# Performance work log

Hardware: AMD Instinct MI355X
Metric: run time of the kernel (lower is better)

Reference implementation:

```python
import jax, jax.numpy as jnp
import numpy as np

H = 12      # num_attention_heads
DH = 64     # attention_head_size
D = H * DH  # hidden_size = 768
EPS = 1e-12

def setup_inputs() -> dict:
    key = jax.random.key(0)
    ks = jax.random.split(key, 12)
    B, S = 8, 1024
    s = 0.02
    return {
        "hidden_states": jax.random.normal(ks[0], (B, S, D), jnp.float32),
        "attention_mask": jnp.zeros((B, 1, 1, S), jnp.float32),
        "Wq": jax.random.normal(ks[1], (D, D), jnp.float32) * s,
        "bq": jnp.zeros((D,), jnp.float32),
        "Wk": jax.random.normal(ks[2], (D, D), jnp.float32) * s,
        "bk": jnp.zeros((D,), jnp.float32),
        "Wv": jax.random.normal(ks[3], (D, D), jnp.float32) * s,
        "bv": jnp.zeros((D,), jnp.float32),
        "Wd": jax.random.normal(ks[4], (D, D), jnp.float32) * s,
        "bd": jnp.zeros((D,), jnp.float32),
        "ln_g": jnp.ones((D,), jnp.float32),
        "ln_b": jnp.zeros((D,), jnp.float32),
    }

def _heads(x, W, b):
    # [B,S,D] -> [B,H,S,Dh]
    B, S, _ = x.shape
    y = x @ W.T + b
    return y.reshape(B, S, H, DH).transpose(0, 2, 1, 3)

def reference(hidden_states, attention_mask, Wq, bq, Wk, bk, Wv, bv, Wd, bd, ln_g, ln_b):
    q = _heads(hidden_states, Wq, bq)
    k = _heads(hidden_states, Wk, bk)
    v = _heads(hidden_states, Wv, bv)
    scores = jnp.einsum('bhqd,bhkd->bhqk', q, k) / np.sqrt(DH).astype(np.float32)
    scores = scores + attention_mask  # broadcast [B,1,1,S]
    probs = jax.nn.softmax(scores, axis=-1)
    ctx = jnp.einsum('bhqk,bhkd->bhqd', probs, v)
    B, _, S, _ = ctx.shape
    ctx = ctx.transpose(0, 2, 1, 3).reshape(B, S, D)
    out = ctx @ Wd.T + bd  # dropout = identity (eval)
    x = hidden_states + out
    mu = jnp.mean(x, axis=-1, keepdims=True)
    var = jnp.var(x, axis=-1, keepdims=True)
    return (x - mu) / jnp.sqrt(var + EPS) * ln_g + ln_b
```

## Files before the change

kernel.cpp:

```cpp
#include <hip/hip_runtime.h>

typedef unsigned short u16;
typedef unsigned int u32;

#define H_ 12
#define DH_ 64
#define D_ 768
#define S_ 1024
#define B_ 8
#define M_TOT 8192
#define LOG2E 1.44269504089f

using f32x4  = __attribute__((ext_vector_type(4))) float;
using bf16x8 = __attribute__((ext_vector_type(8))) short;

__device__ inline u16 f2bf(float f) {
  union { float f; u32 u; } v; v.f = f;
  u32 r = v.u + 0x7FFFu + ((v.u >> 16) & 1u);
  return (u16)(r >> 16);
}

__device__ inline float bf2f(u16 b) {
  union { u32 u; float f; } v; v.u = ((u32)b) << 16;
  return v.f;
}

__device__ inline void gload_lds16(const u16* g, u16* l) {
  __builtin_amdgcn_global_load_lds((const __attribute__((address_space(1))) void*)g,
                                   (__attribute__((address_space(3))) void*)l, 16, 0, 0);
}

__global__ void convert_all(const float* __restrict__ X,
                            const float* __restrict__ Wq, const float* __restrict__ Wk,
                            const float* __restrict__ Wv, const float* __restrict__ Wd,
                            u16* __restrict__ Xb, u16* __restrict__ Wqkv, u16* __restrict__ Wdb) {
  int stride = gridDim.x * blockDim.x;
  int tid = blockIdx.x * blockDim.x + threadIdx.x;
  const int NX4 = M_TOT * D_ / 4;
  const int NW4 = D_ * D_ / 4;
  const int NW = D_ * D_;
  for (int i = tid; i < NX4; i += stride) {
    float4 x = ((const float4*)X)[i];
    uint2 p;
    p.x = (u32)f2bf(x.x) | ((u32)f2bf(x.y) << 16);
    p.y = (u32)f2bf(x.z) | ((u32)f2bf(x.w) << 16);
    ((uint2*)Xb)[i] = p;
  }
  for (int i = tid; i < NW4; i += stride) {
    float4 q = ((const float4*)Wq)[i];
    float4 k = ((const float4*)Wk)[i];
    float4 v = ((const float4*)Wv)[i];
    float4 d = ((const float4*)Wd)[i];
    uint2 pq, pk, pv, pd;
    pq.x = (u32)f2bf(q.x) | ((u32)f2bf(q.y) << 16); pq.y = (u32)f2bf(q.z) | ((u32)f2bf(q.w) << 16);
    pk.x = (u32)f2bf(k.x) | ((u32)f2bf(k.y) << 16); pk.y = (u32)f2bf(k.z) | ((u32)f2bf(k.w) << 16);
    pv.x = (u32)f2bf(v.x) | ((u32)f2bf(v.y) << 16); pv.y = (u32)f2bf(v.z) | ((u32)f2bf(v.w) << 16);
    pd.x = (u32)f2bf(d.x) | ((u32)f2bf(d.y) << 16); pd.y = (u32)f2bf(d.z) | ((u32)f2bf(d.w) << 16);
    ((uint2*)Wqkv)[i]            = pq;
    ((uint2*)(Wqkv + NW))[i]     = pk;
    ((uint2*)(Wqkv + 2*NW))[i]   = pv;
    ((uint2*)Wdb)[i]             = pd;
  }
}

#define NT_ 24

__global__ __launch_bounds__(256, 4) void gemm_qkv(
    const u16* __restrict__ A, const u16* __restrict__ Bw,
    const float* __restrict__ bq, const float* __restrict__ bk, const float* __restrict__ bv,
    u16* __restrict__ Q, u16* __restrict__ K, u16* __restrict__ Vt) {
  __shared__ u16 As[2 * 128 * 32];
  __shared__ u16 Bs[2 * 128 * 32];
  int tid = threadIdx.x, lane = tid & 63, wave = tid >> 6;
  int wg = blockIdx.x;
  int xcd = wg & 7, li = wg >> 3;
  int m0 = (xcd * 8 + (li & 7)) * 128;
  int n0 = (li >> 3) * 128;
  int wm = (wave >> 1) * 64, wn = (wave & 1) * 64;
  int fr = lane & 15, fg = lane >> 4;
  f32x4 acc[4][4] = {};

  int srow = tid >> 2;
  int schunk = (lane & 3) ^ ((lane >> 3) & 3);
  const u16* AgS = A  + (size_t)(m0 + srow) * D_ + schunk * 8;
  const u16* BgS = Bw + (size_t)(n0 + srow) * D_ + schunk * 8;
  u16* Abase = &As[wave * 512];
  u16* Bbase = &Bs[wave * 512];
  int ra = (fg ^ ((fr >> 1) & 3)) * 8;

  gload_lds16(AgS,            Abase);
  gload_lds16(AgS + 64 * D_,  Abase + 2048);
  gload_lds16(BgS,            Bbase);
  gload_lds16(BgS + 64 * D_,  Bbase + 2048);
  __syncthreads();

  for (int t = 0; t < NT_; ++t) {
    int cur = t & 1, nxt = cur ^ 1;
    if (t < NT_ - 1) {
      int k1 = (t + 1) * 32;
      gload_lds16(AgS + k1,           Abase + nxt * 4096);
      gload_lds16(AgS + 64 * D_ + k1, Abase + nxt * 4096 + 2048);
      gload_lds16(BgS + k1,           Bbase + nxt * 4096);
      gload_lds16(BgS + 64 * D_ + k1, Bbase + nxt * 4096 + 2048);
    }
    bf16x8 af[4], bf[4];
#pragma unroll
    for (int i = 0; i < 4; i++) {
      af[i] = *(const bf16x8*)&As[cur * 4096 + (wm + i * 16 + fr) * 32 + ra];
      bf[i] = *(const bf16x8*)&Bs[cur * 4096 + (wn + i * 16 + fr) * 32 + ra];
    }
    __builtin_amdgcn_s_setprio(1);
#pragma unroll
    for (int mi = 0; mi < 4; mi++)
#pragma unroll
      for (int ni = 0; ni < 4; ni++)
        acc[mi][ni] = __builtin_amdgcn_mfma_f32_16x16x32_bf16(af[mi], bf[ni], acc[mi][ni], 0, 0, 0);
    __builtin_amdgcn_s_setprio(0);
    __syncthreads();
  }

  int which = n0 / D_;
  int ncol0 = n0 % D_;
  const float* bias = (which == 0) ? bq : (which == 1) ? bk : bv;
  if (which == 2) {
#pragma unroll
    for (int mi = 0; mi < 4; mi++)
#pragma unroll
      for (int ni = 0; ni < 4; ni++) {
        int col = ncol0 + wn + ni*16 + fr;
        float bb = bias[col];
        int row = m0 + wm + mi*16 + fg*4;
        int bidx = row >> 10, s = row & 1023;
        int hh = col >> 6, dd = col & 63;
        u16 t0 = f2bf(acc[mi][ni][0] + bb);
        u16 t1 = f2bf(acc[mi][ni][1] + bb);
        u16 t2 = f2bf(acc[mi][ni][2] + bb);
        u16 t3 = f2bf(acc[mi][ni][3] + bb);
        uint2 pk2;
        pk2.x = (u32)t0 | ((u32)t1 << 16);
        pk2.y = (u32)t2 | ((u32)t3 << 16);
        *(uint2*)(Vt + ((size_t)((bidx * H_ + hh) * DH_ + dd)) * S_ + s) = pk2;
      }
  } else {
    u16* Out = (which == 0) ? Q : K;
    float scale = (which == 0) ? (0.125f * LOG2E) : 1.0f;
#pragma unroll
    for (int mi = 0; mi < 4; mi++)
#pragma unroll
      for (int ni = 0; ni < 4; ni++) {
        int col = ncol0 + wn + ni*16 + fr;
        float bb = bias[col];
#pragma unroll
        for (int r = 0; r < 4; r++) {
          int row = m0 + wm + mi*16 + fg*4 + r;
          Out[row * D_ + col] = f2bf((acc[mi][ni][r] + bb) * scale);
        }
      }
  }
}

__global__ __launch_bounds__(256, 4) void gemm_out(
    const u16* __restrict__ A, const u16* __restrict__ Bw,
    const float* __restrict__ bd, const float* __restrict__ hidden,
    u16* __restrict__ Tmp) {
  __shared__ u16 As[2 * 64 * 32];
  __shared__ u16 Bs[2 * 128 * 32];
  int tid = threadIdx.x, lane = tid & 63, wave = tid >> 6;
  int wg = blockIdx.x;
  int xcd = wg & 7, li = wg >> 3;
  int m0 = (xcd * 16 + (li & 15)) * 64;
  int n0 = (li >> 4) * 128;
  int wm = (wave >> 1) * 32, wn = (wave & 1) * 64;
  int fr = lane & 15, fg = lane >> 4;
  f32x4 acc[2][4] = {};

  int srow = tid >> 2;
  int schunk = (lane & 3) ^ ((lane >> 3) & 3);
  const u16* AgS = A  + (size_t)(m0 + srow) * D_ + schunk * 8;
  const u16* BgS = Bw + (size_t)(n0 + srow) * D_ + schunk * 8;
  u16* Abase = &As[wave * 512];
  u16* Bbase = &Bs[wave * 512];
  int ra = (fg ^ ((fr >> 1) & 3)) * 8;

  gload_lds16(AgS,            Abase);
  gload_lds16(BgS,            Bbase);
  gload_lds16(BgS + 64 * D_,  Bbase + 2048);
  __syncthreads();

  for (int t = 0; t < NT_; ++t) {
    int cur = t & 1, nxt = cur ^ 1;
    if (t < NT_ - 1) {
      int k1 = (t + 1) * 32;
      gload_lds16(AgS + k1,           Abase + nxt * 2048);
      gload_lds16(BgS + k1,           Bbase + nxt * 4096);
      gload_lds16(BgS + 64 * D_ + k1, Bbase + nxt * 4096 + 2048);
    }
    bf16x8 af[2], bf[4];
#pragma unroll
    for (int i = 0; i < 2; i++)
      af[i] = *(const bf16x8*)&As[cur * 2048 + (wm + i * 16 + fr) * 32 + ra];
#pragma unroll
    for (int i = 0; i < 4; i++)
      bf[i] = *(const bf16x8*)&Bs[cur * 4096 + (wn + i * 16 + fr) * 32 + ra];
    __builtin_amdgcn_s_setprio(1);
#pragma unroll
    for (int mi = 0; mi < 2; mi++)
#pragma unroll
      for (int ni = 0; ni < 4; ni++)
        acc[mi][ni] = __builtin_amdgcn_mfma_f32_16x16x32_bf16(af[mi], bf[ni], acc[mi][ni], 0, 0, 0);
    __builtin_amdgcn_s_setprio(0);
    __syncthreads();
  }

#pragma unroll
  for (int mi = 0; mi < 2; mi++)
#pragma unroll
    for (int ni = 0; ni < 4; ni++) {
      int col = n0 + wn + ni*16 + fr;
      float bb = bd[col];
#pragma unroll
      for (int r = 0; r < 4; r++) {
        int row = m0 + wm + mi*16 + fg*4 + r;
        Tmp[row * D_ + col] = f2bf(acc[mi][ni][r] + bb + hidden[(size_t)row * D_ + col]);
      }
    }
}

__global__ __launch_bounds__(256) void attn_kernel(
    const u16* __restrict__ Q, const u16* __restrict__ K, const u16* __restrict__ Vt,
    const float* __restrict__ mask, u16* __restrict__ Ctx) {
  __shared__ u16 Ks[2][64 * 64];
  __shared__ u16 Vs[2][64 * 64];
  __shared__ u16 Ps[4][16 * 64];
  int tid = threadIdx.x, lane = tid & 63, wave = tid >> 6;
  int i = blockIdx.x;
  int xcd = i & 7, slot = i >> 3;
  int bh = xcd * 12 + (slot >> 3);
  int qt = slot & 7;
  int b = bh / H_, h = bh % H_;
  int q0 = qt * 128 + wave * 32;
  int fr = lane & 15, fg = lane >> 4;

  bf16x8 qf[2][2];
#pragma unroll
  for (int s = 0; s < 2; s++) {
    const u16* Qrow = Q + (size_t)(b * S_ + q0 + s*16 + fr) * D_ + h * DH_;
    qf[s][0] = *(const bf16x8*)(Qrow + fg * 8);
    qf[s][1] = *(const bf16x8*)(Qrow + 32 + fg * 8);
  }

  int srow = tid >> 2;
  int scc = (tid & 3) * 16;
  int sw = (srow & 7) << 3;
  int sidx0 = srow * 64 + (scc ^ sw);
  int sidx1 = srow * 64 + ((scc + 8) ^ sw);
  const u16* Kg0 = K  + (size_t)(b * S_ + srow) * D_ + h * DH_ + scc;
  const u16* Vg0 = Vt + (size_t)(bh * DH_ + srow) * S_ + scc;
  const float* mbase = mask + b * S_;

  int frw = (fr & 7) << 3;
  int rc0 = (fg * 8) ^ frw;
  int rc1 = (32 + fg * 8) ^ frw;
  int pcw[4];
#pragma unroll
  for (int kb = 0; kb < 4; kb++) pcw[kb] = (kb * 16 + fg * 4) ^ frw;

  f32x4 acc[2][4] = {};
  float l_part[2] = {0.f, 0.f};

  int4 kr0 = *(const int4*)Kg0;
  int4 kr1 = *(const int4*)(Kg0 + 8);
  int4 vr0 = *(const int4*)Vg0;
  int4 vr1 = *(const int4*)(Vg0 + 8);
  *(int4*)&Ks[0][sidx0] = kr0; *(int4*)&Ks[0][sidx1] = kr1;
  *(int4*)&Vs[0][sidx0] = vr0; *(int4*)&Vs[0][sidx1] = vr1;
  __syncthreads();

  u16* Pw = Ps[wave];

  for (int t = 0; t < 16; ++t) {
    int cur = t & 1;
    int kt = t * 64;
    if (t < 15) {
      const u16* Kg = Kg0 + (size_t)(kt + 64) * D_;
      const u16* Vg = Vg0 + (kt + 64);
      kr0 = *(const int4*)Kg; kr1 = *(const int4*)(Kg + 8);
      vr0 = *(const int4*)Vg; vr1 = *(const int4*)(Vg + 8);
    }

    f32x4 mv[4];
#pragma unroll
    for (int kb = 0; kb < 4; kb++) {
      float4 m4 = *(const float4*)&mbase[kt + kb*16 + fg*4];
      mv[kb][0] = m4.x * LOG2E; mv[kb][1] = m4.y * LOG2E;
      mv[kb][2] = m4.z * LOG2E; mv[kb][3] = m4.w * LOG2E;
    }

    bf16x8 kf[4][2];
#pragma unroll
    for (int kb = 0; kb < 4; kb++) {
      int r = kb * 16 + fr;
      kf[kb][0] = *(const bf16x8*)&Ks[cur][r * 64 + rc0];
      kf[kb][1] = *(const bf16x8*)&Ks[cur][r * 64 + rc1];
    }

    bf16x8 pf[2][2];
#pragma unroll
    for (int s = 0; s < 2; s++) {
#pragma unroll
      for (int kb = 0; kb < 4; kb++) {
        f32x4 sv = mv[kb];
        sv = __builtin_amdgcn_mfma_f32_16x16x32_bf16(kf[kb][0], qf[s][0], sv, 0, 0, 0);
        sv = __builtin_amdgcn_mfma_f32_16x16x32_bf16(kf[kb][1], qf[s][1], sv, 0, 0, 0);
        float p0 = __builtin_amdgcn_exp2f(sv[0]);
        float p1 = __builtin_amdgcn_exp2f(sv[1]);
        float p2 = __builtin_amdgcn_exp2f(sv[2]);
        float p3 = __builtin_amdgcn_exp2f(sv[3]);
        l_part[s] += (p0 + p1) + (p2 + p3);
        u32 lo, hi;
        asm("v_cvt_pk_bf16_f32 %0, %1, %2" : "=v"(lo) : "v"(p0), "v"(p1));
        asm("v_cvt_pk_bf16_f32 %0, %1, %2" : "=v"(hi) : "v"(p2), "v"(p3));
        uint2 pk2; pk2.x = lo; pk2.y = hi;
        *(uint2*)&Pw[fr * 64 + pcw[kb]] = pk2;
      }
      pf[s][0] = *(const bf16x8*)&Pw[fr * 64 + rc0];
      pf[s][1] = *(const bf16x8*)&Pw[fr * 64 + rc1];
    }

    __builtin_amdgcn_s_setprio(1);
#pragma unroll
    for (int ns = 0; ns < 4; ns++) {
      int r = ns * 16 + fr;
      bf16x8 vf0 = *(const bf16x8*)&Vs[cur][r * 64 + rc0];
      bf16x8 vf1 = *(const bf16x8*)&Vs[cur][r * 64 + rc1];
#pragma unroll
      for (int s = 0; s < 2; s++) {
        acc[s][ns] = __builtin_amdgcn_mfma_f32_16x16x32_bf16(pf[s][0], vf0, acc[s][ns], 0, 0, 0);
        acc[s][ns] = __builtin_amdgcn_mfma_f32_16x16x32_bf16(pf[s][1], vf1, acc[s][ns], 0, 0, 0);
      }
    }
    __builtin_amdgcn_s_setprio(0);

    if (t < 15) {
      int nxt = cur ^ 1;
      *(int4*)&Ks[nxt][sidx0] = kr0; *(int4*)&Ks[nxt][sidx1] = kr1;
      *(int4*)&Vs[nxt][sidx0] = vr0; *(int4*)&Vs[nxt][sidx1] = vr1;
      __syncthreads();
    }
  }

  float li[2][4];
#pragma unroll
  for (int s = 0; s < 2; s++) {
    l_part[s] += __shfl_xor(l_part[s], 16);
    l_part[s] += __shfl_xor(l_part[s], 32);
    float inv = 1.0f / l_part[s];
#pragma unroll
    for (int r = 0; r < 4; r++)
      li[s][r] = __shfl(inv, fg*4 + r);
  }
#pragma unroll
  for (int s = 0; s < 2; s++) {
    u16* Crow = Ctx + (size_t)(b * S_ + q0 + s*16) * D_ + h * DH_;
#pragma unroll
    for (int ns = 0; ns < 4; ns++)
#pragma unroll
      for (int r = 0; r < 4; r++)
        Crow[(fg*4 + r) * D_ + ns*16 + fr] = f2bf(acc[s][ns][r] * li[s][r]);
  }
}

__global__ __launch_bounds__(256) void ln_kernel(
    const u16* __restrict__ Tmp, const float* __restrict__ g,
    const float* __restrict__ bta, float* __restrict__ out) {
  int wave = threadIdx.x >> 6, lane = threadIdx.x & 63;
  int row = blockIdx.x * 4 + wave;
  const uint2* x2 = (const uint2*)(Tmp + (size_t)row * D_);
  const float4* g4 = (const float4*)g;
  const float4* b4 = (const float4*)bta;
  float4* o4 = (float4*)(out + (size_t)row * D_);
  float v[3][4];
  float s = 0.f, s2 = 0.f;
#pragma unroll
  for (int w = 0; w < 3; w++) {
    uint2 raw = x2[lane + w * 64];
    v[w][0] = bf2f((u16)(raw.x & 0xFFFF));
    v[w][1] = bf2f((u16)(raw.x >> 16));
    v[w][2] = bf2f((u16)(raw.y & 0xFFFF));
    v[w][3] = bf2f((u16)(raw.y >> 16));
#pragma unroll
    for (int e = 0; e < 4; e++) { s += v[w][e]; s2 += v[w][e] * v[w][e]; }
  }
#pragma unroll
  for (int m = 1; m < 64; m <<= 1) { s += __shfl_xor(s, m); s2 += __shfl_xor(s2, m); }
  float mean = s * (1.0f / D_);
  float var = s2 * (1.0f / D_) - mean * mean;
  float inv = rsqrtf(var + 1e-12f);
#pragma unroll
  for (int w = 0; w < 3; w++) {
    float4 gg = g4[lane + w * 64];
    float4 bb = b4[lane + w * 64];
    float4 o;
    o.x = (v[w][0] - mean) * inv * gg.x + bb.x;
    o.y = (v[w][1] - mean) * inv * gg.y + bb.y;
    o.z = (v[w][2] - mean) * inv * gg.z + bb.z;
    o.w = (v[w][3] - mean) * inv * gg.w + bb.w;
    o4[lane + w * 64] = o;
  }
}

extern "C" void kernel_launch(void* const* d_in, const int* in_sizes, int n_in,
                              void* d_out, int out_size, void* d_ws, size_t ws_size,
                              hipStream_t stream) {
  (void)in_sizes; (void)n_in; (void)out_size; (void)ws_size;
  const float* hidden = (const float*)d_in[0];
  const float* mask   = (const float*)d_in[1];
  const float* Wq = (const float*)d_in[2];
  const float* bq = (const float*)d_in[3];
  const float* Wk = (const float*)d_in[4];
  const float* bk = (const float*)d_in[5];
  const float* Wv = (const float*)d_in[6];
  const float* bv = (const float*)d_in[7];
  const float* Wd = (const float*)d_in[8];
  const float* bd = (const float*)d_in[9];
  const float* ln_g = (const float*)d_in[10];
  const float* ln_b = (const float*)d_in[11];
  float* out = (float*)d_out;

  char* ws = (char*)d_ws;
  u16* Xb    = (u16*)(ws);
  u16* Wqkv  = (u16*)(ws + 12582912);
  u16* Wdb   = (u16*)(ws + 16121856);
  u16* Q     = (u16*)(ws + 17301504);
  u16* K     = (u16*)(ws + 29884416);
  u16* Vt    = (u16*)(ws + 42467328);
  u16* Ctx   = (u16*)(ws + 55050240);
  u16* Tmp   = (u16*)(ws + 17301504);

  convert_all<<<2048, 256, 0, stream>>>(hidden, Wq, Wk, Wv, Wd, Xb, Wqkv, Wdb);
  gemm_qkv<<<1152, 256, 0, stream>>>(Xb, Wqkv, bq, bk, bv, Q, K, Vt);
  attn_kernel<<<768, 256, 0, stream>>>(Q, K, Vt, mask, Ctx);
  gemm_out<<<768, 256, 0, stream>>>(Ctx, Wdb, bd, hidden, Tmp);
  ln_kernel<<<2048, 256, 0, stream>>>(Tmp, ln_g, ln_b, out);
}
```

Measured before the change: 127.9 us.

## Halve attention query tile per block and stage scaled mask in shared memory

Each attention block now handles 64 queries (16 per wave) instead of 128, doubling the grid to 1536 blocks for better occupancy and CU balance. The mask row is preloaded into shared memory once, pre-scaled by log2e, instead of being read from global each tile. The trade-off is that each block reuses its loaded K/V tiles for half as many queries, so total K/V global traffic doubles. Register pressure per wave drops, which may let more waves stay resident.

```diff
diff --git a/kernel.cpp b/kernel.cpp
--- a/kernel.cpp
+++ b/kernel.cpp
@@ -232,22 +232,25 @@
   __shared__ u16 Ks[2][64 * 64];
   __shared__ u16 Vs[2][64 * 64];
   __shared__ u16 Ps[4][16 * 64];
+  __shared__ float Ms[S_];
   int tid = threadIdx.x, lane = tid & 63, wave = tid >> 6;
   int i = blockIdx.x;
   int xcd = i & 7, slot = i >> 3;
-  int bh = xcd * 12 + (slot >> 3);
-  int qt = slot & 7;
+  int bh = xcd * 12 + (slot >> 4);
+  int qt = slot & 15;
   int b = bh / H_, h = bh % H_;
-  int q0 = qt * 128 + wave * 32;
+  int q0 = qt * 64 + wave * 16;
   int fr = lane & 15, fg = lane >> 4;
 
-  bf16x8 qf[2][2];
-#pragma unroll
-  for (int s = 0; s < 2; s++) {
-    const u16* Qrow = Q + (size_t)(b * S_ + q0 + s*16 + fr) * D_ + h * DH_;
-    qf[s][0] = *(const bf16x8*)(Qrow + fg * 8);
-    qf[s][1] = *(const bf16x8*)(Qrow + 32 + fg * 8);
-  }
+  {
+    float4 m4 = ((const float4*)(mask + b * S_))[tid];
+    m4.x *= LOG2E; m4.y *= LOG2E; m4.z *= LOG2E; m4.w *= LOG2E;
+    ((float4*)Ms)[tid] = m4;
+  }
+
+  const u16* Qrow = Q + (size_t)(b * S_ + q0 + fr) * D_ + h * DH_;
+  bf16x8 qf0 = *(const bf16x8*)(Qrow + fg * 8);
+  bf16x8 qf1 = *(const bf16x8*)(Qrow + 32 + fg * 8);
 
   int srow = tid >> 2;
   int scc = (tid & 3) * 16;
@@ -256,7 +259,6 @@
   int sidx1 = srow * 64 + ((scc + 8) ^ sw);
   const u16* Kg0 = K  + (size_t)(b * S_ + srow) * D_ + h * DH_ + scc;
   const u16* Vg0 = Vt + (size_t)(bh * DH_ + srow) * S_ + scc;
-  const float* mbase = mask + b * S_;
 
   int frw = (fr & 7) << 3;
   int rc0 = (fg * 8) ^ frw;
@@ -265,8 +267,8 @@
 #pragma unroll
   for (int kb = 0; kb < 4; kb++) pcw[kb] = (kb * 16 + fg * 4) ^ frw;
 
-  f32x4 acc[2][4] = {};
-  float l_part[2] = {0.f, 0.f};
+  f32x4 acc[4] = {};
+  float l_part = 0.f;
 
   int4 kr0 = *(const int4*)Kg0;
   int4 kr1 = *(const int4*)(Kg0 + 8);
@@ -288,44 +290,28 @@
       vr0 = *(const int4*)Vg; vr1 = *(const int4*)(Vg + 8);
     }
 
-    f32x4 mv[4];
-#pragma unroll
-    for (int kb = 0; kb < 4; kb++) {
-      float4 m4 = *(const float4*)&mbase[kt + kb*16 + fg*4];
-      mv[kb][0] = m4.x * LOG2E; mv[kb][1] = m4.y * LOG2E;
-      mv[kb][2] = m4.z * LOG2E; mv[kb][3] = m4.w * LOG2E;
-    }
-
-    bf16x8 kf[4][2];
 #pragma unroll
     for (int kb = 0; kb < 4; kb++) {
       int r = kb * 16 + fr;
-      kf[kb][0] = *(const bf16x8*)&Ks[cur][r * 64 + rc0];
-      kf[kb][1] = *(const bf16x8*)&Ks[cur][r * 64 + rc1];
-    }
-
-    bf16x8 pf[2][2];
-#pragma unroll
-    for (int s = 0; s < 2; s++) {
-#pragma unroll
-      for (int kb = 0; kb < 4; kb++) {
-        f32x4 sv = mv[kb];
-        sv = __builtin_amdgcn_mfma_f32_16x16x32_bf16(kf[kb][0], qf[s][0], sv, 0, 0, 0);
-        sv = __builtin_amdgcn_mfma_f32_16x16x32_bf16(kf[kb][1], qf[s][1], sv, 0, 0, 0);
-        float p0 = __builtin_amdgcn_exp2f(sv[0]);
-        float p1 = __builtin_amdgcn_exp2f(sv[1]);
-        float p2 = __builtin_amdgcn_exp2f(sv[2]);
-        float p3 = __builtin_amdgcn_exp2f(sv[3]);
-        l_part[s] += (p0 + p1) + (p2 + p3);
-        u32 lo, hi;
-        asm("v_cvt_pk_bf16_f32 %0, %1, %2" : "=v"(lo) : "v"(p0), "v"(p1));
-        asm("v_cvt_pk_bf16_f32 %0, %1, %2" : "=v"(hi) : "v"(p2), "v"(p3));
-        uint2 pk2; pk2.x = lo; pk2.y = hi;
-        *(uint2*)&Pw[fr * 64 + pcw[kb]] = pk2;
-      }
-      pf[s][0] = *(const bf16x8*)&Pw[fr * 64 + rc0];
-      pf[s][1] = *(const bf16x8*)&Pw[fr * 64 + rc1];
-    }
+      bf16x8 kf0 = *(const bf16x8*)&Ks[cur][r * 64 + rc0];
+      bf16x8 kf1 = *(const bf16x8*)&Ks[cur][r * 64 + rc1];
+      float4 m4 = *(const float4*)&Ms[kt + kb*16 + fg*4];
+      f32x4 sv; sv[0] = m4.x; sv[1] = m4.y; sv[2] = m4.z; sv[3] = m4.w;
+      sv = __builtin_amdgcn_mfma_f32_16x16x32_bf16(kf0, qf0, sv, 0, 0, 0);
+      sv = __builtin_amdgcn_mfma_f32_16x16x32_bf16(kf1, qf1, sv, 0, 0, 0);
+      float p0 = __builtin_amdgcn_exp2f(sv[0]);
+      float p1 = __builtin_amdgcn_exp2f(sv[1]);
+      float p2 = __builtin_amdgcn_exp2f(sv[2]);
+      float p3 = __builtin_amdgcn_exp2f(sv[3]);
+      l_part += (p0 + p1) + (p2 + p3);
+      u32 lo, hi;
+      asm("v_cvt_pk_bf16_f32 %0, %1, %2" : "=v"(lo) : "v"(p0), "v"(p1));
+      asm("v_cvt_pk_bf16_f32 %0, %1, %2" : "=v"(hi) : "v"(p2), "v"(p3));
+      uint2 pk2; pk2.x = lo; pk2.y = hi;
+      *(uint2*)&Pw[fr * 64 + pcw[kb]] = pk2;
+    }
+    bf16x8 pf0 = *(const bf16x8*)&Pw[fr * 64 + rc0];
+    bf16x8 pf1 = *(const bf16x8*)&Pw[fr * 64 + rc1];
 
     __builtin_amdgcn_s_setprio(1);
 #pragma unroll
@@ -333,11 +319,8 @@
       int r = ns * 16 + fr;
       bf16x8 vf0 = *(const bf16x8*)&Vs[cur][r * 64 + rc0];
       bf16x8 vf1 = *(const bf16x8*)&Vs[cur][r * 64 + rc1];
-#pragma unroll
-      for (int s = 0; s < 2; s++) {
-        acc[s][ns] = __builtin_amdgcn_mfma_f32_16x16x32_bf16(pf[s][0], vf0, acc[s][ns], 0, 0, 0);
-        acc[s][ns] = __builtin_amdgcn_mfma_f32_16x16x32_bf16(pf[s][1], vf1, acc[s][ns], 0, 0, 0);
-      }
+      acc[ns] = __builtin_amdgcn_mfma_f32_16x16x32_bf16(pf0, vf0, acc[ns], 0, 0, 0);
+      acc[ns] = __builtin_amdgcn_mfma_f32_16x16x32_bf16(pf1, vf1, acc[ns], 0, 0, 0);
     }
     __builtin_amdgcn_s_setprio(0);
 
@@ -349,25 +332,20 @@
     }
   }
 
-  float li[2][4];
-#pragma unroll
-  for (int s = 0; s < 2; s++) {
-    l_part[s] += __shfl_xor(l_part[s], 16);
-    l_part[s] += __shfl_xor(l_part[s], 32);
-    float inv = 1.0f / l_part[s];
+  l_part += __shfl_xor(l_part, 16);
+  l_part += __shfl_xor(l_part, 32);
+  float inv = 1.0f / l_part;
+  float li[4];
+#pragma unroll
+  for (int r = 0; r < 4; r++)
+    li[r] = __shfl(inv, fg*4 + r);
+
+  u16* Crow = Ctx + (size_t)(b * S_ + q0) * D_ + h * DH_;
+#pragma unroll
+  for (int ns = 0; ns < 4; ns++)
 #pragma unroll
     for (int r = 0; r < 4; r++)
-      li[s][r] = __shfl(inv, fg*4 + r);
-  }
-#pragma unroll
-  for (int s = 0; s < 2; s++) {
-    u16* Crow = Ctx + (size_t)(b * S_ + q0 + s*16) * D_ + h * DH_;
-#pragma unroll
-    for (int ns = 0; ns < 4; ns++)
-#pragma unroll
-      for (int r = 0; r < 4; r++)
-        Crow[(fg*4 + r) * D_ + ns*16 + fr] = f2bf(acc[s][ns][r] * li[s][r]);
-  }
+      Crow[(fg*4 + r) * D_ + ns*16 + fr] = f2bf(acc[ns][r] * li[r]);
 }
 
 __global__ __launch_bounds__(256) void ln_kernel(
@@ -439,7 +417,7 @@
 
   convert_all<<<2048, 256, 0, stream>>>(hidden, Wq, Wk, Wv, Wd, Xb, Wqkv, Wdb);
   gemm_qkv<<<1152, 256, 0, stream>>>(Xb, Wqkv, bq, bk, bv, Q, K, Vt);
-  attn_kernel<<<768, 256, 0, stream>>>(Q, K, Vt, mask, Ctx);
+  attn_kernel<<<1536, 256, 0, stream>>>(Q, K, Vt, mask, Ctx);
   gemm_out<<<768, 256, 0, stream>>>(Ctx, Wdb, bd, hidden, Tmp);
   ln_kernel<<<2048, 256, 0, stream>>>(Tmp, ln_g, ln_b, out);
 }
```

After: 129.2 us. No clear change (+1.0%).
